# Optimization experiments

Hardware: AMD Instinct MI355X
Metric: run time of the kernel (lower is better)

## Reference

```python
import jax, jax.numpy as jnp
import numpy as np

ALPHA = 4.0          # init alpha
THRESH = 0.693       # validity threshold (~ln 2) from the torch code
K = 8                # instances per class (labels are grouped in blocks of K)
N = 2048
D = 512
NUM_CLASSES = N // K


def setup_inputs() -> dict:
    key = jax.random.key(0)
    inputs = jax.random.normal(key, (N, D), dtype=jnp.float32)
    # grouped labels: [0]*K, [1]*K, ... (required by the original masked_select/resize logic)
    targets = jnp.repeat(jnp.arange(NUM_CLASSES, dtype=jnp.int32), K)
    return {"inputs": inputs, "targets": targets}


def reference(inputs, targets):
    n = inputs.shape[0]
    # x = alpha * L2-normalize(inputs)
    x = ALPHA * inputs / jnp.linalg.norm(inputs, axis=1, keepdims=True)
    # squared euclidean distance matrix [n, n]
    sq = jnp.sum(x * x, axis=1, keepdims=True)
    dist = sq + sq.T - 2.0 * (x @ x.T)

    eye = jnp.eye(n, dtype=bool)
    same = targets[:, None] == targets[None, :]
    pos_mask = same & ~eye            # positives (excluding self)
    neg_mask = ~same                  # negatives

    m = K - 1                         # positives per row
    n_neg = n - K                     # negatives per row
    # stable argsort puts True (0 after ~) positions first, preserving row-major order
    pos_idx = jnp.argsort(~pos_mask, axis=1)[:, :m]
    neg_idx = jnp.argsort(~neg_mask, axis=1)[:, :n_neg]
    pos_dist = jnp.take_along_axis(dist, pos_idx, axis=1)   # [n, m]
    neg_dist = jnp.take_along_axis(dist, neg_idx, axis=1)   # [n, n_neg]

    # triplet_mat[i, j, k] = log(exp(pos[i,k] - neg[i,j]) + 1)
    trip = jnp.log1p(jnp.exp(pos_dist[:, None, :] - neg_dist[:, :, None]))  # [n, n_neg, m]
    valid = trip > THRESH
    cnt = jnp.sum(valid, axis=(1, 2))                        # valid triplets per row
    row_sum = jnp.sum(jnp.where(valid, trip, 0.0), axis=(1, 2))
    row_mean = jnp.where(cnt > 0, row_sum / jnp.maximum(cnt, 1), 0.0)
    total = jnp.sum(cnt)
    loss = jnp.where(total > 0, jnp.sum(row_mean) / total, 0.0)

    accuracy = jnp.mean((cnt == 0).astype(jnp.float32))
    pos_d = jnp.mean(pos_dist)
    neg_d = jnp.mean(neg_dist)
    return loss, accuracy, pos_d, neg_d
```

## Files before the change

### kernel.cpp

```cpp
#include <hip/hip_runtime.h>
#include <hip/hip_bf16.h>
#include <math.h>

#define N 2048
#define D 512
#define KC 8
#define M (KC - 1)
#define NNEG (N - KC)
#define ALPHA 4.0f
#define THRESH 0.693f
#define LN2F 0.6931471805599453f
#define INV_LN2F 1.4426950408889634f
#define C2 (THRESH * INV_LN2F)

typedef unsigned short ushort_t;
using frag_ab = __attribute__((ext_vector_type(8))) short;
using frag_cd = __attribute__((ext_vector_type(4))) float;

__global__ __launch_bounds__(128) void normalize_kernel(const float* __restrict__ in,
                                                        ushort_t* __restrict__ xb,
                                                        float* __restrict__ sq) {
    int row = blockIdx.x;
    int tid = threadIdx.x;
    const float* r = in + (size_t)row * D;
    float p = 0.f;
    for (int d = tid; d < D; d += 128) { float v = r[d]; p += v * v; }
    __shared__ float red[128];
    red[tid] = p; __syncthreads();
    for (int s = 64; s > 0; s >>= 1) { if (tid < s) red[tid] += red[tid + s]; __syncthreads(); }
    float scale = ALPHA / sqrtf(red[0]);
    __syncthreads();
    float q = 0.f;
    for (int d = tid; d < D; d += 128) {
        float v = r[d] * scale;
        q += v * v;
        __hip_bfloat16 h = __float2bfloat16(v);
        xb[(size_t)row * D + d] = *(ushort_t*)&h;
    }
    red[tid] = q; __syncthreads();
    for (int s = 64; s > 0; s >>= 1) { if (tid < s) red[tid] += red[tid + s]; __syncthreads(); }
    if (tid == 0) sq[row] = red[0];
}

#define TM 128
#define TN 128
#define TK 32

__global__ __launch_bounds__(256) void gemm_dist_mfma(const ushort_t* __restrict__ xb,
                                                      const float* __restrict__ sq,
                                                      float* __restrict__ dist) {
    __shared__ ushort_t As[TM * TK];
    __shared__ ushort_t Bs[TN * TK];
    int tid  = threadIdx.x;
    int lane = tid & 63;
    int w    = tid >> 6;
    int wm   = w >> 1, wn = w & 1;
    int quad = lane >> 4, l16 = lane & 15;
    int bi = blockIdx.y, bj = blockIdx.x;

    frag_cd acc[4][4];
    #pragma unroll
    for (int i = 0; i < 4; ++i)
        #pragma unroll
        for (int j = 0; j < 4; ++j)
            acc[i][j] = (frag_cd){0.f, 0.f, 0.f, 0.f};

    int c0 = tid, c1 = 256 + tid;
    int r0 = c0 >> 2, s0 = (c0 & 3) * 8;
    int r1 = c1 >> 2, s1 = (c1 & 3) * 8;
    const ushort_t* gA0 = xb + (size_t)(bi * TM + r0) * D + s0;
    const ushort_t* gA1 = xb + (size_t)(bi * TM + r1) * D + s1;
    const ushort_t* gB0 = xb + (size_t)(bj * TN + r0) * D + s0;
    const ushort_t* gB1 = xb + (size_t)(bj * TN + r1) * D + s1;
    ushort_t* lA0 = As + (size_t)c0 * 8;
    ushort_t* lA1 = As + (size_t)c1 * 8;
    ushort_t* lB0 = Bs + (size_t)c0 * 8;
    ushort_t* lB1 = Bs + (size_t)c1 * 8;

    int aoff[4], boff[4];
    #pragma unroll
    for (int i = 0; i < 4; ++i) {
        aoff[i] = (wm * 64 + i * 16 + l16) * TK + quad * 8;
        boff[i] = (wn * 64 + i * 16 + l16) * TK + quad * 8;
    }

    for (int k0 = 0; k0 < D; k0 += TK) {
        __builtin_amdgcn_global_load_lds((const __attribute__((address_space(1))) unsigned int*)(gA0 + k0),
                                         (__attribute__((address_space(3))) unsigned int*)lA0, 16, 0, 0);
        __builtin_amdgcn_global_load_lds((const __attribute__((address_space(1))) unsigned int*)(gA1 + k0),
                                         (__attribute__((address_space(3))) unsigned int*)lA1, 16, 0, 0);
        __builtin_amdgcn_global_load_lds((const __attribute__((address_space(1))) unsigned int*)(gB0 + k0),
                                         (__attribute__((address_space(3))) unsigned int*)lB0, 16, 0, 0);
        __builtin_amdgcn_global_load_lds((const __attribute__((address_space(1))) unsigned int*)(gB1 + k0),
                                         (__attribute__((address_space(3))) unsigned int*)lB1, 16, 0, 0);
        __syncthreads();

        frag_ab a[4], b[4];
        #pragma unroll
        for (int i = 0; i < 4; ++i) {
            a[i] = *(const frag_ab*)&As[aoff[i]];
            b[i] = *(const frag_ab*)&Bs[boff[i]];
        }
        #pragma unroll
        for (int i = 0; i < 4; ++i)
            #pragma unroll
            for (int j = 0; j < 4; ++j)
                acc[i][j] = __builtin_amdgcn_mfma_f32_16x16x32_bf16(a[i], b[j], acc[i][j], 0, 0, 0);
        __syncthreads();
    }

    int row_base = bi * TM + wm * 64 + quad * 4;
    int col_base = bj * TN + wn * 64 + l16;
    #pragma unroll
    for (int j = 0; j < 4; ++j) {
        int col = col_base + j * 16;
        float sjv = sq[col];
        #pragma unroll
        for (int i = 0; i < 4; ++i) {
            int row = row_base + i * 16;
            #pragma unroll
            for (int r = 0; r < 4; ++r) {
                dist[(size_t)(row + r) * N + col] = sq[row + r] + sjv - 2.f * acc[i][j][r];
            }
        }
    }
}

__global__ __launch_bounds__(256) void triplet_kernel(const float* __restrict__ dist,
                                                      float4* __restrict__ rowres) {
    int i = blockIdx.x;
    int tid = threadIdx.x;
    int cs = (i >> 3) << 3;
    const float* drow = dist + (size_t)i * N;

    __shared__ float pos[M];
    if (tid == 0) {
        int c = 0;
        for (int j = cs; j < cs + KC; ++j)
            if (j != i) pos[c++] = drow[j];
    }
    __syncthreads();
    float p[M], ep[M];
    #pragma unroll
    for (int k = 0; k < M; ++k) { p[k] = pos[k]; ep[k] = __expf(p[k]); }

    float s2 = 0.f, nsum = 0.f;
    unsigned cnt = 0;
    for (int j = tid; j < N; j += 256) {
        if (j >= cs && j < cs + KC) continue;
        float neg = drow[j];
        nsum += neg;
        float en = __expf(-neg);
        #pragma unroll
        for (int k = 0; k < M; ++k) {
            float e = ep[k] * en;
            float l = __log2f(1.f + e);
            if (l > C2) { cnt++; s2 += l; }
        }
    }

    __shared__ float rs[256];
    __shared__ float rn[256];
    __shared__ unsigned rc[256];
    rs[tid] = s2; rn[tid] = nsum; rc[tid] = cnt;
    __syncthreads();
    for (int st = 128; st > 0; st >>= 1) {
        if (tid < st) { rs[tid] += rs[tid + st]; rn[tid] += rn[tid + st]; rc[tid] += rc[tid + st]; }
        __syncthreads();
    }
    if (tid == 0) {
        float psum = 0.f;
        #pragma unroll
        for (int k = 0; k < M; ++k) psum += p[k];
        rowres[i] = make_float4(rs[0], (float)rc[0], psum, rn[0]);
    }
}

__global__ __launch_bounds__(256) void final_reduce_kernel(const float4* __restrict__ rowres,
                                                           float* __restrict__ out) {
    int tid = threadIdx.x;
    double srm = 0.0, ps = 0.0, ns = 0.0;
    unsigned long long tot = 0; unsigned zr = 0;
    for (int i = tid; i < N; i += 256) {
        float4 r = rowres[i];
        unsigned c = (unsigned)r.y;
        if (c > 0) {
            float row_mean = r.x * LN2F / (float)c;
            srm += (double)row_mean;
            tot += c;
        } else {
            zr++;
        }
        ps += (double)r.z;
        ns += (double)r.w;
    }
    __shared__ double d0[256], d1[256], d2[256];
    __shared__ unsigned long long dt[256];
    __shared__ unsigned dz[256];
    d0[tid] = srm; d1[tid] = ps; d2[tid] = ns; dt[tid] = tot; dz[tid] = zr;
    __syncthreads();
    for (int st = 128; st > 0; st >>= 1) {
        if (tid < st) {
            d0[tid] += d0[tid + st]; d1[tid] += d1[tid + st]; d2[tid] += d2[tid + st];
            dt[tid] += dt[tid + st]; dz[tid] += dz[tid + st];
        }
        __syncthreads();
    }
    if (tid == 0) {
        unsigned long long total = dt[0];
        out[0] = (total > 0) ? (float)(d0[0] / (double)total) : 0.f;
        out[1] = (float)((double)dz[0] / (double)N);
        out[2] = (float)(d1[0] / (double)((size_t)N * M));
        out[3] = (float)(d2[0] / (double)((size_t)N * NNEG));
    }
}

extern "C" void kernel_launch(void* const* d_in, const int* in_sizes, int n_in,
                              void* d_out, int out_size, void* d_ws, size_t ws_size,
                              hipStream_t stream) {
    const float* inputs = (const float*)d_in[0];
    float* out = (float*)d_out;
    char* ws = (char*)d_ws;

    const size_t off_xb   = 0;
    const size_t off_sq   = off_xb + (size_t)N * D * sizeof(ushort_t);
    const size_t off_dist = off_sq + (size_t)N * sizeof(float) + 4096;
    const size_t off_row  = off_dist + (size_t)N * N * sizeof(float);
    const size_t needed   = off_row + (size_t)N * sizeof(float4);
    if (ws_size < needed) return;

    ushort_t* xb     = (ushort_t*)(ws + off_xb);
    float*    sq     = (float*)(ws + off_sq);
    float*    dist   = (float*)(ws + off_dist);
    float4*   rowres = (float4*)(ws + off_row);

    normalize_kernel<<<N, 128, 0, stream>>>(inputs, xb, sq);
    gemm_dist_mfma<<<dim3(N / TN, N / TM), 256, 0, stream>>>(xb, sq, dist);
    triplet_kernel<<<N, 256, 0, stream>>>(dist, rowres);
    final_reduce_kernel<<<1, 256, 0, stream>>>(rowres, out);
}
```

Before: 95.70 us.

## Fuse triplet loss into distance GEMM epilogue, drop dist matrix round-trip

Removes the 16MB distance matrix write and re-read by computing the triplet log1p terms directly in the GEMM epilogue. Each row-block writes per-column-tile partial sums, which the final reduce combines. A new small kernel precomputes positive distances and their exponentials per class with scalar bf16 dot products. The change also double-buffers the GEMM's LDS tiles and vectorizes normalization with wave shuffles. The triplet math now runs spread over GEMM tiles instead of per-row blocks, so total transcendental work is unchanged but overlaps better; positive distances come from a different code path, which may differ slightly numerically.

Measured after the change: 105.7 us. +10.4%, slower.

```diff
diff --git a/kernel.cpp b/kernel.cpp
--- a/kernel.cpp
+++ b/kernel.cpp
@@ -17,46 +17,117 @@
 using frag_ab = __attribute__((ext_vector_type(8))) short;
 using frag_cd = __attribute__((ext_vector_type(4))) float;
 
+__device__ __forceinline__ void gload16(const ushort_t* g, ushort_t* l) {
+    __builtin_amdgcn_global_load_lds((const __attribute__((address_space(1))) unsigned int*)g,
+                                     (__attribute__((address_space(3))) unsigned int*)l, 16, 0, 0);
+}
+
 __global__ __launch_bounds__(128) void normalize_kernel(const float* __restrict__ in,
                                                         ushort_t* __restrict__ xb,
                                                         float* __restrict__ sq) {
     int row = blockIdx.x;
     int tid = threadIdx.x;
-    const float* r = in + (size_t)row * D;
-    float p = 0.f;
-    for (int d = tid; d < D; d += 128) { float v = r[d]; p += v * v; }
-    __shared__ float red[128];
-    red[tid] = p; __syncthreads();
-    for (int s = 64; s > 0; s >>= 1) { if (tid < s) red[tid] += red[tid + s]; __syncthreads(); }
-    float scale = ALPHA / sqrtf(red[0]);
-    __syncthreads();
-    float q = 0.f;
-    for (int d = tid; d < D; d += 128) {
-        float v = r[d] * scale;
-        q += v * v;
-        __hip_bfloat16 h = __float2bfloat16(v);
-        xb[(size_t)row * D + d] = *(ushort_t*)&h;
-    }
-    red[tid] = q; __syncthreads();
-    for (int s = 64; s > 0; s >>= 1) { if (tid < s) red[tid] += red[tid + s]; __syncthreads(); }
-    if (tid == 0) sq[row] = red[0];
+    const float4* r4 = (const float4*)(in + (size_t)row * D);
+    float4 v = r4[tid];
+    float p = v.x * v.x + v.y * v.y + v.z * v.z + v.w * v.w;
+    #pragma unroll
+    for (int m = 1; m < 64; m <<= 1) p += __shfl_xor(p, m);
+    __shared__ float sred[2];
+    if ((tid & 63) == 0) sred[tid >> 6] = p;
+    __syncthreads();
+    float scale = ALPHA / sqrtf(sred[0] + sred[1]);
+    float4 w = make_float4(v.x * scale, v.y * scale, v.z * scale, v.w * scale);
+    float q = w.x * w.x + w.y * w.y + w.z * w.z + w.w * w.w;
+    __hip_bfloat16 h0 = __float2bfloat16(w.x);
+    __hip_bfloat16 h1 = __float2bfloat16(w.y);
+    __hip_bfloat16 h2 = __float2bfloat16(w.z);
+    __hip_bfloat16 h3 = __float2bfloat16(w.w);
+    ushort4 u;
+    u.x = *(ushort_t*)&h0; u.y = *(ushort_t*)&h1; u.z = *(ushort_t*)&h2; u.w = *(ushort_t*)&h3;
+    ((ushort4*)(xb + (size_t)row * D))[tid] = u;
+    #pragma unroll
+    for (int m = 1; m < 64; m <<= 1) q += __shfl_xor(q, m);
+    __syncthreads();
+    if ((tid & 63) == 0) sred[tid >> 6] = q;
+    __syncthreads();
+    if (tid == 0) sq[row] = sred[0] + sred[1];
+}
+
+#define DP (D + 8)
+__global__ __launch_bounds__(64) void posdist_kernel(const ushort_t* __restrict__ xb,
+                                                     const float* __restrict__ sq,
+                                                     float* __restrict__ eprow) {
+    int cls = blockIdx.x;
+    int tid = threadIdx.x;
+    int base = cls * KC;
+    __shared__ ushort_t xl[KC][DP];
+    const uint4* src = (const uint4*)(xb + (size_t)base * D);
+    #pragma unroll
+    for (int c8 = 0; c8 < 8; ++c8) {
+        int c = c8 * 64 + tid;
+        int r = c >> 6, off = c & 63;
+        *(uint4*)&xl[r][off * 8] = src[c];
+    }
+    __syncthreads();
+    int i = tid >> 3, j = tid & 7;
+    const ushort_t* ri = xl[i];
+    const ushort_t* rj = xl[j];
+    float acc = 0.f;
+    #pragma unroll 2
+    for (int d = 0; d < D; d += 8) {
+        uint4 ui = *(const uint4*)&ri[d];
+        uint4 uj = *(const uint4*)&rj[d];
+        unsigned a0 = ui.x, a1 = ui.y, a2 = ui.z, a3 = ui.w;
+        unsigned b0 = uj.x, b1 = uj.y, b2 = uj.z, b3 = uj.w;
+        acc += __uint_as_float(a0 << 16) * __uint_as_float(b0 << 16);
+        acc += __uint_as_float(a0 & 0xffff0000u) * __uint_as_float(b0 & 0xffff0000u);
+        acc += __uint_as_float(a1 << 16) * __uint_as_float(b1 << 16);
+        acc += __uint_as_float(a1 & 0xffff0000u) * __uint_as_float(b1 & 0xffff0000u);
+        acc += __uint_as_float(a2 << 16) * __uint_as_float(b2 << 16);
+        acc += __uint_as_float(a2 & 0xffff0000u) * __uint_as_float(b2 & 0xffff0000u);
+        acc += __uint_as_float(a3 << 16) * __uint_as_float(b3 << 16);
+        acc += __uint_as_float(a3 & 0xffff0000u) * __uint_as_float(b3 & 0xffff0000u);
+    }
+    float dij = sq[base + i] + sq[base + j] - 2.f * acc;
+    float pc = (i == j) ? 0.f : dij;
+    #pragma unroll
+    for (int m = 1; m < 8; m <<= 1) pc += __shfl_xor(pc, m);
+    if (i != j) {
+        int k = j - (j > i ? 1 : 0);
+        eprow[(size_t)(base + i) * 8 + k] = __expf(dij);
+    }
+    if (j == 0) eprow[(size_t)(base + i) * 8 + 7] = pc;
 }
 
 #define TM 128
 #define TN 128
 #define TK 32
-
-__global__ __launch_bounds__(256) void gemm_dist_mfma(const ushort_t* __restrict__ xb,
-                                                      const float* __restrict__ sq,
-                                                      float* __restrict__ dist) {
-    __shared__ ushort_t As[TM * TK];
-    __shared__ ushort_t Bs[TN * TK];
+#define NT (D / TK)
+
+__global__ __launch_bounds__(256) void fused_dist_triplet(const ushort_t* __restrict__ xb,
+                                                          const float* __restrict__ sq,
+                                                          const float* __restrict__ eprow,
+                                                          float4* __restrict__ partial) {
+    __shared__ ushort_t As[2 * TM * TK];
+    __shared__ ushort_t Bs[2 * TN * TK];
+    __shared__ float eps_lds[TM][8];
+    __shared__ float sqr_lds[TM];
+    __shared__ float sqc_lds[TN];
+    __shared__ float4 comb[2][TM];
+
     int tid  = threadIdx.x;
     int lane = tid & 63;
     int w    = tid >> 6;
     int wm   = w >> 1, wn = w & 1;
     int quad = lane >> 4, l16 = lane & 15;
     int bi = blockIdx.y, bj = blockIdx.x;
+
+    {
+        int rr = tid >> 1, half = (tid & 1) * 4;
+        *(float4*)&eps_lds[rr][half] = *(const float4*)(eprow + (size_t)(bi * TM + rr) * 8 + half);
+    }
+    if (tid < TM) sqr_lds[tid] = sq[bi * TM + tid];
+    else          sqc_lds[tid - TM] = sq[bj * TN + (tid - TM)];
 
     frag_cd acc[4][4];
     #pragma unroll
@@ -72,10 +143,10 @@
     const ushort_t* gA1 = xb + (size_t)(bi * TM + r1) * D + s1;
     const ushort_t* gB0 = xb + (size_t)(bj * TN + r0) * D + s0;
     const ushort_t* gB1 = xb + (size_t)(bj * TN + r1) * D + s1;
-    ushort_t* lA0 = As + (size_t)c0 * 8;
-    ushort_t* lA1 = As + (size_t)c1 * 8;
-    ushort_t* lB0 = Bs + (size_t)c0 * 8;
-    ushort_t* lB1 = Bs + (size_t)c1 * 8;
+    ushort_t* lA0 = As + c0 * 8;
+    ushort_t* lA1 = As + c1 * 8;
+    ushort_t* lB0 = Bs + c0 * 8;
+    ushort_t* lB1 = Bs + c1 * 8;
 
     int aoff[4], boff[4];
     #pragma unroll
@@ -84,120 +155,111 @@
         boff[i] = (wn * 64 + i * 16 + l16) * TK + quad * 8;
     }
 
-    for (int k0 = 0; k0 < D; k0 += TK) {
-        __builtin_amdgcn_global_load_lds((const __attribute__((address_space(1))) unsigned int*)(gA0 + k0),
-                                         (__attribute__((address_space(3))) unsigned int*)lA0, 16, 0, 0);
-        __builtin_amdgcn_global_load_lds((const __attribute__((address_space(1))) unsigned int*)(gA1 + k0),
-                                         (__attribute__((address_space(3))) unsigned int*)lA1, 16, 0, 0);
-        __builtin_amdgcn_global_load_lds((const __attribute__((address_space(1))) unsigned int*)(gB0 + k0),
-                                         (__attribute__((address_space(3))) unsigned int*)lB0, 16, 0, 0);
-        __builtin_amdgcn_global_load_lds((const __attribute__((address_space(1))) unsigned int*)(gB1 + k0),
-                                         (__attribute__((address_space(3))) unsigned int*)lB1, 16, 0, 0);
+    gload16(gA0, lA0); gload16(gA1, lA1); gload16(gB0, lB0); gload16(gB1, lB1);
+    int cur = 0;
+    for (int t = 0; t < NT; ++t) {
         __syncthreads();
-
+        if (t + 1 < NT) {
+            int k0 = (t + 1) * TK;
+            int bo = (cur ^ 1) * TM * TK;
+            gload16(gA0 + k0, lA0 + bo);
+            gload16(gA1 + k0, lA1 + bo);
+            gload16(gB0 + k0, lB0 + bo);
+            gload16(gB1 + k0, lB1 + bo);
+        }
+        const ushort_t* Ab = As + cur * TM * TK;
+        const ushort_t* Bb = Bs + cur * TN * TK;
         frag_ab a[4], b[4];
         #pragma unroll
         for (int i = 0; i < 4; ++i) {
-            a[i] = *(const frag_ab*)&As[aoff[i]];
-            b[i] = *(const frag_ab*)&Bs[boff[i]];
+            a[i] = *(const frag_ab*)(Ab + aoff[i]);
+            b[i] = *(const frag_ab*)(Bb + boff[i]);
         }
         #pragma unroll
         for (int i = 0; i < 4; ++i)
             #pragma unroll
             for (int j = 0; j < 4; ++j)
                 acc[i][j] = __builtin_amdgcn_mfma_f32_16x16x32_bf16(a[i], b[j], acc[i][j], 0, 0, 0);
-        __syncthreads();
-    }
-
-    int row_base = bi * TM + wm * 64 + quad * 4;
-    int col_base = bj * TN + wn * 64 + l16;
-    #pragma unroll
-    for (int j = 0; j < 4; ++j) {
-        int col = col_base + j * 16;
-        float sjv = sq[col];
-        #pragma unroll
-        for (int i = 0; i < 4; ++i) {
-            int row = row_base + i * 16;
+        cur ^= 1;
+    }
+
+    float sjv[4];
+    #pragma unroll
+    for (int j = 0; j < 4; ++j) sjv[j] = sqc_lds[wn * 64 + j * 16 + l16];
+    int colbase = bj * TN + wn * 64 + l16;
+    int lr0 = wm * 64 + quad * 4;
+    #pragma unroll
+    for (int i = 0; i < 4; ++i) {
+        #pragma unroll
+        for (int r = 0; r < 4; ++r) {
+            int lr  = lr0 + i * 16 + r;
+            int row = bi * TM + lr;
+            int cs  = row & ~(KC - 1);
+            float sr = sqr_lds[lr];
+            float4 e0 = *(float4*)&eps_lds[lr][0];
+            float4 e1 = *(float4*)&eps_lds[lr][4];
+            float epv[7] = {e0.x, e0.y, e0.z, e0.w, e1.x, e1.y, e1.z};
+            float s2 = 0.f, ns = 0.f;
+            int cnt = 0;
             #pragma unroll
-            for (int r = 0; r < 4; ++r) {
-                dist[(size_t)(row + r) * N + col] = sq[row + r] + sjv - 2.f * acc[i][j][r];
+            for (int j = 0; j < 4; ++j) {
+                int col = colbase + j * 16;
+                if ((unsigned)(col - cs) >= (unsigned)KC) {
+                    float neg = sr + sjv[j] - 2.f * acc[i][j][r];
+                    ns += neg;
+                    float en = __expf(-neg);
+                    #pragma unroll
+                    for (int k = 0; k < 7; ++k) {
+                        float l = __log2f(1.f + epv[k] * en);
+                        if (l > C2) { cnt++; s2 += l; }
+                    }
+                }
             }
-        }
-    }
-}
-
-__global__ __launch_bounds__(256) void triplet_kernel(const float* __restrict__ dist,
-                                                      float4* __restrict__ rowres) {
-    int i = blockIdx.x;
-    int tid = threadIdx.x;
-    int cs = (i >> 3) << 3;
-    const float* drow = dist + (size_t)i * N;
-
-    __shared__ float pos[M];
-    if (tid == 0) {
-        int c = 0;
-        for (int j = cs; j < cs + KC; ++j)
-            if (j != i) pos[c++] = drow[j];
-    }
-    __syncthreads();
-    float p[M], ep[M];
-    #pragma unroll
-    for (int k = 0; k < M; ++k) { p[k] = pos[k]; ep[k] = __expf(p[k]); }
-
-    float s2 = 0.f, nsum = 0.f;
-    unsigned cnt = 0;
-    for (int j = tid; j < N; j += 256) {
-        if (j >= cs && j < cs + KC) continue;
-        float neg = drow[j];
-        nsum += neg;
-        float en = __expf(-neg);
-        #pragma unroll
-        for (int k = 0; k < M; ++k) {
-            float e = ep[k] * en;
-            float l = __log2f(1.f + e);
-            if (l > C2) { cnt++; s2 += l; }
-        }
-    }
-
-    __shared__ float rs[256];
-    __shared__ float rn[256];
-    __shared__ unsigned rc[256];
-    rs[tid] = s2; rn[tid] = nsum; rc[tid] = cnt;
-    __syncthreads();
-    for (int st = 128; st > 0; st >>= 1) {
-        if (tid < st) { rs[tid] += rs[tid + st]; rn[tid] += rn[tid + st]; rc[tid] += rc[tid + st]; }
-        __syncthreads();
-    }
-    if (tid == 0) {
-        float psum = 0.f;
-        #pragma unroll
-        for (int k = 0; k < M; ++k) psum += p[k];
-        rowres[i] = make_float4(rs[0], (float)rc[0], psum, rn[0]);
-    }
-}
-
-__global__ __launch_bounds__(256) void final_reduce_kernel(const float4* __restrict__ rowres,
+            #pragma unroll
+            for (int m = 1; m < 16; m <<= 1) {
+                s2  += __shfl_xor(s2, m);
+                ns  += __shfl_xor(ns, m);
+                cnt += __shfl_xor(cnt, m);
+            }
+            if (l16 == 0) comb[wn][lr] = make_float4(s2, (float)cnt, ns, 0.f);
+        }
+    }
+    __syncthreads();
+    if (tid < TM) {
+        float4 a0 = comb[0][tid], b0 = comb[1][tid];
+        partial[(size_t)bj * N + bi * TM + tid] =
+            make_float4(a0.x + b0.x, a0.y + b0.y, a0.z + b0.z, 0.f);
+    }
+}
+
+__global__ __launch_bounds__(256) void final_reduce_kernel(const float4* __restrict__ partial,
+                                                           const float* __restrict__ eprow,
                                                            float* __restrict__ out) {
     int tid = threadIdx.x;
-    double srm = 0.0, ps = 0.0, ns = 0.0;
+    double srm = 0.0, ps = 0.0, nsd = 0.0;
     unsigned long long tot = 0; unsigned zr = 0;
     for (int i = tid; i < N; i += 256) {
-        float4 r = rowres[i];
-        unsigned c = (unsigned)r.y;
+        float s2 = 0.f, cf = 0.f, nsum = 0.f;
+        #pragma unroll
+        for (int b = 0; b < 16; ++b) {
+            float4 pp = partial[(size_t)b * N + i];
+            s2 += pp.x; cf += pp.y; nsum += pp.z;
+        }
+        unsigned c = (unsigned)cf;
         if (c > 0) {
-            float row_mean = r.x * LN2F / (float)c;
+            float row_mean = s2 * LN2F / (float)c;
             srm += (double)row_mean;
             tot += c;
         } else {
             zr++;
         }
-        ps += (double)r.z;
-        ns += (double)r.w;
+        ps  += (double)eprow[(size_t)i * 8 + 7];
+        nsd += (double)nsum;
     }
     __shared__ double d0[256], d1[256], d2[256];
     __shared__ unsigned long long dt[256];
     __shared__ unsigned dz[256];
-    d0[tid] = srm; d1[tid] = ps; d2[tid] = ns; dt[tid] = tot; dz[tid] = zr;
+    d0[tid] = srm; d1[tid] = ps; d2[tid] = nsd; dt[tid] = tot; dz[tid] = zr;
     __syncthreads();
     for (int st = 128; st > 0; st >>= 1) {
         if (tid < st) {
@@ -222,20 +284,20 @@
     float* out = (float*)d_out;
     char* ws = (char*)d_ws;
 
-    const size_t off_xb   = 0;
-    const size_t off_sq   = off_xb + (size_t)N * D * sizeof(ushort_t);
-    const size_t off_dist = off_sq + (size_t)N * sizeof(float) + 4096;
-    const size_t off_row  = off_dist + (size_t)N * N * sizeof(float);
-    const size_t needed   = off_row + (size_t)N * sizeof(float4);
+    const size_t off_xb = 0;
+    const size_t off_sq = off_xb + (size_t)N * D * sizeof(ushort_t);
+    const size_t off_ep = off_sq + (size_t)N * sizeof(float);
+    const size_t off_pp = off_ep + (size_t)N * 8 * sizeof(float);
+    const size_t needed = off_pp + (size_t)16 * N * sizeof(float4);
     if (ws_size < needed) return;
 
     ushort_t* xb     = (ushort_t*)(ws + off_xb);
     float*    sq     = (float*)(ws + off_sq);
-    float*    dist   = (float*)(ws + off_dist);
-    float4*   rowres = (float4*)(ws + off_row);
+    float*    eprow  = (float*)(ws + off_ep);
+    float4*   partial = (float4*)(ws + off_pp);
 
     normalize_kernel<<<N, 128, 0, stream>>>(inputs, xb, sq);
-    gemm_dist_mfma<<<dim3(N / TN, N / TM), 256, 0, stream>>>(xb, sq, dist);
-    triplet_kernel<<<N, 256, 0, stream>>>(dist, rowres);
-    final_reduce_kernel<<<1, 256, 0, stream>>>(rowres, out);
-}
+    posdist_kernel<<<N / KC, 64, 0, stream>>>(xb, sq, eprow);
+    fused_dist_triplet<<<dim3(N / TN, N / TM), 256, 0, stream>>>(xb, sq, eprow, partial);
+    final_reduce_kernel<<<1, 256, 0, stream>>>(partial, eprow, out);
+}
```

## Shrink distance GEMM tiles to 64x64 and double-buffer LDS loads

Applied to the files above, without the earlier changes.

The distance GEMM moves from 128x128 to 64x64 output tiles, giving four times as many workgroups to spread across the CUs. It also double-buffers the shared-memory A/B tiles, prefetching the next K-slice with global_load_lds while MFMAs run on the current one, so each iteration needs one barrier instead of two. The cost is less data reuse per tile and more total global traffic. Whether the prefetch really overlaps depends on how the compiler places its waitcnt instructions.

Result: faster. 92.30 us (-3.6%).

```diff
diff --git a/kernel.cpp b/kernel.cpp
--- a/kernel.cpp
+++ b/kernel.cpp
@@ -16,6 +16,11 @@
 typedef unsigned short ushort_t;
 using frag_ab = __attribute__((ext_vector_type(8))) short;
 using frag_cd = __attribute__((ext_vector_type(4))) float;
+
+__device__ __forceinline__ void gload16(const ushort_t* g, ushort_t* l) {
+    __builtin_amdgcn_global_load_lds((const __attribute__((address_space(1))) unsigned int*)g,
+                                     (__attribute__((address_space(3))) unsigned int*)l, 16, 0, 0);
+}
 
 __global__ __launch_bounds__(128) void normalize_kernel(const float* __restrict__ in,
                                                         ushort_t* __restrict__ xb,
@@ -42,15 +47,16 @@
     if (tid == 0) sq[row] = red[0];
 }
 
-#define TM 128
-#define TN 128
+#define TM 64
+#define TN 64
 #define TK 32
+#define NT (D / TK)
 
 __global__ __launch_bounds__(256) void gemm_dist_mfma(const ushort_t* __restrict__ xb,
                                                       const float* __restrict__ sq,
                                                       float* __restrict__ dist) {
-    __shared__ ushort_t As[TM * TK];
-    __shared__ ushort_t Bs[TN * TK];
+    __shared__ ushort_t As[2 * TM * TK];
+    __shared__ ushort_t Bs[2 * TN * TK];
     int tid  = threadIdx.x;
     int lane = tid & 63;
     int w    = tid >> 6;
@@ -58,65 +64,60 @@
     int quad = lane >> 4, l16 = lane & 15;
     int bi = blockIdx.y, bj = blockIdx.x;
 
-    frag_cd acc[4][4];
-    #pragma unroll
-    for (int i = 0; i < 4; ++i)
-        #pragma unroll
-        for (int j = 0; j < 4; ++j)
+    frag_cd acc[2][2];
+    #pragma unroll
+    for (int i = 0; i < 2; ++i)
+        #pragma unroll
+        for (int j = 0; j < 2; ++j)
             acc[i][j] = (frag_cd){0.f, 0.f, 0.f, 0.f};
 
-    int c0 = tid, c1 = 256 + tid;
-    int r0 = c0 >> 2, s0 = (c0 & 3) * 8;
-    int r1 = c1 >> 2, s1 = (c1 & 3) * 8;
-    const ushort_t* gA0 = xb + (size_t)(bi * TM + r0) * D + s0;
-    const ushort_t* gA1 = xb + (size_t)(bi * TM + r1) * D + s1;
-    const ushort_t* gB0 = xb + (size_t)(bj * TN + r0) * D + s0;
-    const ushort_t* gB1 = xb + (size_t)(bj * TN + r1) * D + s1;
-    ushort_t* lA0 = As + (size_t)c0 * 8;
-    ushort_t* lA1 = As + (size_t)c1 * 8;
-    ushort_t* lB0 = Bs + (size_t)c0 * 8;
-    ushort_t* lB1 = Bs + (size_t)c1 * 8;
-
-    int aoff[4], boff[4];
-    #pragma unroll
-    for (int i = 0; i < 4; ++i) {
-        aoff[i] = (wm * 64 + i * 16 + l16) * TK + quad * 8;
-        boff[i] = (wn * 64 + i * 16 + l16) * TK + quad * 8;
-    }
-
-    for (int k0 = 0; k0 < D; k0 += TK) {
-        __builtin_amdgcn_global_load_lds((const __attribute__((address_space(1))) unsigned int*)(gA0 + k0),
-                                         (__attribute__((address_space(3))) unsigned int*)lA0, 16, 0, 0);
-        __builtin_amdgcn_global_load_lds((const __attribute__((address_space(1))) unsigned int*)(gA1 + k0),
-                                         (__attribute__((address_space(3))) unsigned int*)lA1, 16, 0, 0);
-        __builtin_amdgcn_global_load_lds((const __attribute__((address_space(1))) unsigned int*)(gB0 + k0),
-                                         (__attribute__((address_space(3))) unsigned int*)lB0, 16, 0, 0);
-        __builtin_amdgcn_global_load_lds((const __attribute__((address_space(1))) unsigned int*)(gB1 + k0),
-                                         (__attribute__((address_space(3))) unsigned int*)lB1, 16, 0, 0);
+    int r0 = tid >> 2, s0 = (tid & 3) * 8;
+    const ushort_t* gA = xb + (size_t)(bi * TM + r0) * D + s0;
+    const ushort_t* gB = xb + (size_t)(bj * TN + r0) * D + s0;
+    ushort_t* lA = As + tid * 8;
+    ushort_t* lB = Bs + tid * 8;
+
+    int aoff[2], boff[2];
+    #pragma unroll
+    for (int i = 0; i < 2; ++i) {
+        aoff[i] = (wm * 32 + i * 16 + l16) * TK + quad * 8;
+        boff[i] = (wn * 32 + i * 16 + l16) * TK + quad * 8;
+    }
+
+    gload16(gA, lA); gload16(gB, lB);
+    int cur = 0;
+    for (int t = 0; t < NT; ++t) {
         __syncthreads();
-
-        frag_ab a[4], b[4];
-        #pragma unroll
-        for (int i = 0; i < 4; ++i) {
-            a[i] = *(const frag_ab*)&As[aoff[i]];
-            b[i] = *(const frag_ab*)&Bs[boff[i]];
-        }
-        #pragma unroll
-        for (int i = 0; i < 4; ++i)
+        if (t + 1 < NT) {
+            int k0 = (t + 1) * TK;
+            int bo = (cur ^ 1) * TM * TK;
+            gload16(gA + k0, lA + bo);
+            gload16(gB + k0, lB + bo);
+        }
+        const ushort_t* Ab = As + cur * TM * TK;
+        const ushort_t* Bb = Bs + cur * TN * TK;
+        frag_ab a[2], b[2];
+        #pragma unroll
+        for (int i = 0; i < 2; ++i) {
+            a[i] = *(const frag_ab*)(Ab + aoff[i]);
+            b[i] = *(const frag_ab*)(Bb + boff[i]);
+        }
+        #pragma unroll
+        for (int i = 0; i < 2; ++i)
             #pragma unroll
-            for (int j = 0; j < 4; ++j)
+            for (int j = 0; j < 2; ++j)
                 acc[i][j] = __builtin_amdgcn_mfma_f32_16x16x32_bf16(a[i], b[j], acc[i][j], 0, 0, 0);
-        __syncthreads();
-    }
-
-    int row_base = bi * TM + wm * 64 + quad * 4;
-    int col_base = bj * TN + wn * 64 + l16;
-    #pragma unroll
-    for (int j = 0; j < 4; ++j) {
+        cur ^= 1;
+    }
+
+    int row_base = bi * TM + wm * 32 + quad * 4;
+    int col_base = bj * TN + wn * 32 + l16;
+    #pragma unroll
+    for (int j = 0; j < 2; ++j) {
         int col = col_base + j * 16;
         float sjv = sq[col];
         #pragma unroll
-        for (int i = 0; i < 4; ++i) {
+        for (int i = 0; i < 2; ++i) {
             int row = row_base + i * 16;
             #pragma unroll
             for (int r = 0; r < 4; ++r) {
```
